# Optimization experiments

Measured on AMD Instinct MI355X. Metric: run time of the kernel, lower is better.

The kernel has to match this reference:

```python
import jax, jax.numpy as jnp
import numpy as np

N_NODES = 10000
N_EDGES = 640000
N_GRAPHS = 64
IN_FEATS = 128
H_FEATS = 128


def setup_inputs() -> dict:
    key = jax.random.key(0)
    ks = jax.random.split(key, 8)
    in_feat = jax.random.normal(ks[0], (N_NODES, IN_FEATS), dtype=jnp.float32)
    src = jax.random.randint(ks[1], (N_EDGES,), 0, N_NODES, dtype=jnp.int32)
    dst = jax.random.randint(ks[2], (N_EDGES,), 0, N_NODES, dtype=jnp.int32)
    graph_ids = jnp.sort(jax.random.randint(ks[3], (N_NODES,), 0, N_GRAPHS, dtype=jnp.int32))
    s1 = 1.0 / np.sqrt(IN_FEATS)
    s2 = 1.0 / np.sqrt(H_FEATS)
    W1 = jax.random.uniform(ks[4], (IN_FEATS, H_FEATS), jnp.float32, -s1, s1)
    b1 = jnp.zeros((H_FEATS,), jnp.float32)
    W2 = jax.random.uniform(ks[5], (H_FEATS, H_FEATS), jnp.float32, -s2, s2)
    b2 = jnp.zeros((H_FEATS,), jnp.float32)
    Wd = jax.random.uniform(ks[6], (H_FEATS, 1), jnp.float32, -s2, s2)
    bd = jnp.zeros((1,), jnp.float32)
    return {"in_feat": in_feat, "src": src, "dst": dst, "graph_ids": graph_ids,
            "W1": W1, "b1": b1, "W2": W2, "b2": b2, "Wd": Wd, "bd": bd}


def _graph_conv(x, src, dst, norm_src, norm_dst, W, b):
    # DGL GraphConv, norm='both': D_dst^{-1/2} A D_src^{-1/2} X W + b
    x = x * norm_src[:, None]
    agg = jax.ops.segment_sum(x[src], dst, num_segments=N_NODES)  # scatter-add over edges
    agg = agg * norm_dst[:, None]
    return agg @ W + b


def reference(in_feat, src, dst, graph_ids, W1, b1, W2, b2, Wd, bd):
    ones_e = jnp.ones((N_EDGES,), in_feat.dtype)
    out_deg = jax.ops.segment_sum(ones_e, src, num_segments=N_NODES)
    in_deg = jax.ops.segment_sum(ones_e, dst, num_segments=N_NODES)
    norm_src = jnp.where(out_deg > 0, out_deg, 1.0) ** -0.5
    norm_dst = jnp.where(in_deg > 0, in_deg, 1.0) ** -0.5

    h = jax.nn.relu(_graph_conv(in_feat, src, dst, norm_src, norm_dst, W1, b1))
    h = jax.nn.relu(_graph_conv(h, src, dst, norm_src, norm_dst, W2, b2))

    # dgl.mean_nodes: per-graph mean of node features
    counts = jax.ops.segment_sum(jnp.ones((N_NODES,), h.dtype), graph_ids, num_segments=N_GRAPHS)
    pooled = jax.ops.segment_sum(h, graph_ids, num_segments=N_GRAPHS)
    pooled = pooled / jnp.maximum(counts, 1.0)[:, None]

    out = pooled @ Wd + bd  # [G, 1]
    return out.squeeze(-1)
```

## Files before the change

kernel.cpp:

```cpp
#include <hip/hip_runtime.h>
#include <hip/hip_fp16.h>

#define N_NODES 10000
#define N_EDGES 640000
#define N_GRAPHS 64
#define FEATS 128

#define NSLICE 128
#define EPS (N_EDGES / NSLICE)
#define CAP 128
#define PRE_BLOCKS 1250

static inline size_t align_up(size_t x, size_t a) { return (x + a - 1) & ~(a - 1); }

__global__ __launch_bounds__(256) void hist_kernel(const int* __restrict__ src,
                                                   const int* __restrict__ dst,
                                                   unsigned short* __restrict__ counts,
                                                   unsigned short* __restrict__ scounts,
                                                   int* __restrict__ graph_cnt,
                                                   float* __restrict__ graph_sum) {
    __shared__ int h[N_NODES];
    const int tid = threadIdx.x;
    const int b = blockIdx.x;
    if (b == 0 && tid < 2 * N_GRAPHS) {
        if (tid < N_GRAPHS) graph_cnt[tid] = 0;
        else                graph_sum[tid - N_GRAPHS] = 0.f;
    }
    const bool is_dst = (b < NSLICE);
    const int slice = is_dst ? b : b - NSLICE;
    const int* col = is_dst ? dst : src;
    unsigned short* outp = (is_dst ? counts : scounts) + slice * N_NODES;

    for (int i = tid; i < N_NODES; i += 256) h[i] = 0;
    __syncthreads();
    const int4* c4 = (const int4*)(col + slice * EPS);
    for (int i = tid; i < EPS / 4; i += 256) {
        int4 v = c4[i];
        atomicAdd(&h[v.x], 1);
        atomicAdd(&h[v.y], 1);
        atomicAdd(&h[v.z], 1);
        atomicAdd(&h[v.w], 1);
    }
    __syncthreads();
    for (int i = tid; i < N_NODES; i += 256) outp[i] = (unsigned short)h[i];
}

__global__ __launch_bounds__(64) void degnorm_base_kernel(const unsigned short* __restrict__ counts,
                                                          const unsigned short* __restrict__ scounts,
                                                          const int* __restrict__ gids,
                                                          int* __restrict__ bases,
                                                          int* __restrict__ deg_in,
                                                          float* __restrict__ norm_src,
                                                          float* __restrict__ norm_dst,
                                                          int* __restrict__ graph_cnt) {
    __shared__ int gcnt[N_GRAPHS];
    const int tid = threadIdx.x;
    gcnt[tid] = 0;
    __syncthreads();
    int n = blockIdx.x * 64 + tid;
    if (n < N_NODES) {
        int run = n * CAP;
        for (int s = 0; s < NSLICE; s++) {
            int c = counts[s * N_NODES + n];
            bases[s * N_NODES + n] = run;
            run += c;
        }
        int di = run - n * CAP;
        int dou = 0;
        for (int s = 0; s < NSLICE; s++) dou += scounts[s * N_NODES + n];
        deg_in[n] = di;
        norm_dst[n] = rsqrtf((float)(di < 1 ? 1 : di));
        norm_src[n] = rsqrtf((float)(dou < 1 ? 1 : dou));
        atomicAdd(&gcnt[gids[n]], 1);
    }
    __syncthreads();
    if (gcnt[tid]) atomicAdd(&graph_cnt[tid], gcnt[tid]);
}

__global__ __launch_bounds__(256) void scatter_prescale_kernel(const int* __restrict__ src,
                                                               const int* __restrict__ dst,
                                                               const int* __restrict__ bases,
                                                               int* __restrict__ sorted_src,
                                                               const float* __restrict__ in_feat,
                                                               const float* __restrict__ norm_src,
                                                               __half* __restrict__ xs) {
    const int tid = threadIdx.x;
    if (blockIdx.x < NSLICE) {
        __shared__ int cur[N_NODES];
        const int s = blockIdx.x;
        for (int i = tid; i < N_NODES; i += 256) cur[i] = bases[s * N_NODES + i];
        __syncthreads();
        const int4* s4 = (const int4*)(src + s * EPS);
        const int4* d4 = (const int4*)(dst + s * EPS);
        for (int i = tid; i < EPS / 4; i += 256) {
            int4 sv = s4[i];
            int4 dv = d4[i];
            int p;
            p = atomicAdd(&cur[dv.x], 1); sorted_src[p] = sv.x;
            p = atomicAdd(&cur[dv.y], 1); sorted_src[p] = sv.y;
            p = atomicAdd(&cur[dv.z], 1); sorted_src[p] = sv.z;
            p = atomicAdd(&cur[dv.w], 1); sorted_src[p] = sv.w;
        }
    } else {
        int i = (blockIdx.x - NSLICE) * 256 + tid;
        if (i < N_NODES * (FEATS / 4)) {
            int n = i >> 5;
            float4 v = ((const float4*)in_feat)[i];
            float s = norm_src[n];
            __half2 h0 = __floats2half2_rn(v.x * s, v.y * s);
            __half2 h1 = __floats2half2_rn(v.z * s, v.w * s);
            __half2* o = (__half2*)(xs + (size_t)i * 4);
            o[0] = h0; o[1] = h1;
        }
    }
}

__device__ __forceinline__ void wave_aggregate(const __half* __restrict__ X,
                                               const int* __restrict__ sorted_src,
                                               const int* __restrict__ deg_in,
                                               const float* __restrict__ norm_dst,
                                               int n, int lane,
                                               float* __restrict__ As_row) {
    const int grp = lane >> 4, l16 = lane & 15;
    const int start = n * CAP;
    const int cnt = deg_in[n];
    const uint4* __restrict__ x4 = (const uint4*)X;
    float acc[8] = {0.f, 0.f, 0.f, 0.f, 0.f, 0.f, 0.f, 0.f};

    int c = grp;
    for (; c + 12 < cnt; c += 16) {
        int idx[4];
#pragma unroll
        for (int k = 0; k < 4; k++) idx[k] = sorted_src[start + c + 4 * k];
        uint4 v[4];
#pragma unroll
        for (int k = 0; k < 4; k++) v[k] = x4[idx[k] * 16 + l16];
#pragma unroll
        for (int k = 0; k < 4; k++) {
            const __half2* hp = (const __half2*)&v[k];
#pragma unroll
            for (int j = 0; j < 4; j++) {
                float2 f = __half22float2(hp[j]);
                acc[2 * j]     += f.x;
                acc[2 * j + 1] += f.y;
            }
        }
    }
    for (; c < cnt; c += 4) {
        uint4 v = x4[sorted_src[start + c] * 16 + l16];
        const __half2* hp = (const __half2*)&v;
#pragma unroll
        for (int j = 0; j < 4; j++) {
            float2 f = __half22float2(hp[j]);
            acc[2 * j]     += f.x;
            acc[2 * j + 1] += f.y;
        }
    }
#pragma unroll
    for (int j = 0; j < 8; j++) {
        acc[j] += __shfl_xor(acc[j], 16);
        acc[j] += __shfl_xor(acc[j], 32);
    }
    if (grp == 0) {
        const float nd = norm_dst[n];
        float4 f0 = make_float4(acc[0] * nd, acc[1] * nd, acc[2] * nd, acc[3] * nd);
        float4 f1 = make_float4(acc[4] * nd, acc[5] * nd, acc[6] * nd, acc[7] * nd);
        *(float4*)(As_row + l16 * 8)     = f0;
        *(float4*)(As_row + l16 * 8 + 4) = f1;
    }
}

__global__ __launch_bounds__(256) void fused_layer1_kernel(const __half* __restrict__ xs,
                                                           const int* __restrict__ sorted_src,
                                                           const int* __restrict__ deg_in,
                                                           const float* __restrict__ norm_dst,
                                                           const float* __restrict__ W,
                                                           const float* __restrict__ bias,
                                                           const float* __restrict__ scale,
                                                           __half* __restrict__ out) {
    __shared__ float As[16 * FEATS];
    const int tid = threadIdx.x;
    const int nb = blockIdx.x * 16;
    const int wave = tid >> 6, lane = tid & 63;
#pragma unroll
    for (int i = 0; i < 4; i++) {
        int ln = wave * 4 + i;
        wave_aggregate(xs, sorted_src, deg_in, norm_dst, nb + ln, lane, As + ln * FEATS);
    }
    __syncthreads();
    int fg = (tid & 31) << 2;
    int r  = tid >> 5;
    const float* a0p = As + r * FEATS;
    const float* a1p = As + (r + 8) * FEATS;
    float4 acc0 = make_float4(0.f, 0.f, 0.f, 0.f);
    float4 acc1 = make_float4(0.f, 0.f, 0.f, 0.f);
#pragma unroll 4
    for (int k = 0; k < FEATS; k++) {
        float a0 = a0p[k];
        float a1 = a1p[k];
        float4 w = *(const float4*)(W + k * FEATS + fg);
        acc0.x = fmaf(a0, w.x, acc0.x); acc0.y = fmaf(a0, w.y, acc0.y);
        acc0.z = fmaf(a0, w.z, acc0.z); acc0.w = fmaf(a0, w.w, acc0.w);
        acc1.x = fmaf(a1, w.x, acc1.x); acc1.y = fmaf(a1, w.y, acc1.y);
        acc1.z = fmaf(a1, w.z, acc1.z); acc1.w = fmaf(a1, w.w, acc1.w);
    }
    float4 bb = *(const float4*)(bias + fg);
    int gn0 = nb + r, gn1 = nb + r + 8;
    float s0 = scale[gn0], s1 = scale[gn1];
    __half2 h00 = __floats2half2_rn(fmaxf(acc0.x + bb.x, 0.f) * s0,
                                    fmaxf(acc0.y + bb.y, 0.f) * s0);
    __half2 h01 = __floats2half2_rn(fmaxf(acc0.z + bb.z, 0.f) * s0,
                                    fmaxf(acc0.w + bb.w, 0.f) * s0);
    __half2 h10 = __floats2half2_rn(fmaxf(acc1.x + bb.x, 0.f) * s1,
                                    fmaxf(acc1.y + bb.y, 0.f) * s1);
    __half2 h11 = __floats2half2_rn(fmaxf(acc1.z + bb.z, 0.f) * s1,
                                    fmaxf(acc1.w + bb.w, 0.f) * s1);
    __half2* o0 = (__half2*)(out + (size_t)gn0 * FEATS + fg);
    __half2* o1 = (__half2*)(out + (size_t)gn1 * FEATS + fg);
    o0[0] = h00; o0[1] = h01;
    o1[0] = h10; o1[1] = h11;
}

__global__ __launch_bounds__(256) void fused_layer2_kernel(const __half* __restrict__ h,
                                                           const int* __restrict__ sorted_src,
                                                           const int* __restrict__ deg_in,
                                                           const float* __restrict__ norm_dst,
                                                           const float* __restrict__ W,
                                                           const float* __restrict__ bias,
                                                           const float* __restrict__ Wd,
                                                           const int* __restrict__ gids,
                                                           float* __restrict__ graph_sum) {
    __shared__ float As[16 * FEATS];
    __shared__ float bins[N_GRAPHS];
    const int tid = threadIdx.x;
    const int nb = blockIdx.x * 16;
    const int wave = tid >> 6, lane = tid & 63;
    if (tid < N_GRAPHS) bins[tid] = 0.f;
#pragma unroll
    for (int i = 0; i < 4; i++) {
        int ln = wave * 4 + i;
        wave_aggregate(h, sorted_src, deg_in, norm_dst, nb + ln, lane, As + ln * FEATS);
    }
    __syncthreads();
    int fg = (tid & 31) << 2;
    int r  = tid >> 5;
    const float* a0p = As + r * FEATS;
    const float* a1p = As + (r + 8) * FEATS;
    float4 acc0 = make_float4(0.f, 0.f, 0.f, 0.f);
    float4 acc1 = make_float4(0.f, 0.f, 0.f, 0.f);
#pragma unroll 4
    for (int k = 0; k < FEATS; k++) {
        float a0 = a0p[k];
        float a1 = a1p[k];
        float4 w = *(const float4*)(W + k * FEATS + fg);
        acc0.x = fmaf(a0, w.x, acc0.x); acc0.y = fmaf(a0, w.y, acc0.y);
        acc0.z = fmaf(a0, w.z, acc0.z); acc0.w = fmaf(a0, w.w, acc0.w);
        acc1.x = fmaf(a1, w.x, acc1.x); acc1.y = fmaf(a1, w.y, acc1.y);
        acc1.z = fmaf(a1, w.z, acc1.z); acc1.w = fmaf(a1, w.w, acc1.w);
    }
    float4 bb = *(const float4*)(bias + fg);
    float4 wd = *(const float4*)(Wd + fg);
    float p0 = fmaxf(acc0.x + bb.x, 0.f) * wd.x + fmaxf(acc0.y + bb.y, 0.f) * wd.y +
               fmaxf(acc0.z + bb.z, 0.f) * wd.z + fmaxf(acc0.w + bb.w, 0.f) * wd.w;
    float p1 = fmaxf(acc1.x + bb.x, 0.f) * wd.x + fmaxf(acc1.y + bb.y, 0.f) * wd.y +
               fmaxf(acc1.z + bb.z, 0.f) * wd.z + fmaxf(acc1.w + bb.w, 0.f) * wd.w;
#pragma unroll
    for (int d = 16; d >= 1; d >>= 1) {
        p0 += __shfl_down(p0, d);
        p1 += __shfl_down(p1, d);
    }
    if ((tid & 31) == 0) {
        int gn0 = nb + r, gn1 = nb + r + 8;
        atomicAdd(&bins[gids[gn0]], p0);
        atomicAdd(&bins[gids[gn1]], p1);
    }
    __syncthreads();
    if (tid < N_GRAPHS) {
        float v = bins[tid];
        if (v != 0.f) atomicAdd(&graph_sum[tid], v);
    }
}

__global__ __launch_bounds__(64) void final_kernel(const float* __restrict__ graph_sum,
                                                   const int* __restrict__ graph_cnt,
                                                   const float* __restrict__ bd,
                                                   float* __restrict__ out) {
    int g = threadIdx.x;
    if (g < N_GRAPHS) {
        out[g] = graph_sum[g] / fmaxf((float)graph_cnt[g], 1.f) + bd[0];
    }
}

extern "C" void kernel_launch(void* const* d_in, const int* in_sizes, int n_in,
                              void* d_out, int out_size, void* d_ws, size_t ws_size,
                              hipStream_t stream) {
    const float* in_feat = (const float*)d_in[0];
    const int*   src     = (const int*)d_in[1];
    const int*   dst     = (const int*)d_in[2];
    const int*   gids    = (const int*)d_in[3];
    const float* W1      = (const float*)d_in[4];
    const float* b1      = (const float*)d_in[5];
    const float* W2      = (const float*)d_in[6];
    const float* b2      = (const float*)d_in[7];
    const float* Wd      = (const float*)d_in[8];
    const float* bd      = (const float*)d_in[9];
    float* out = (float*)d_out;

    char* ws = (char*)d_ws;
    size_t off = 0;
    int* graph_cnt = (int*)(ws + off); off += N_GRAPHS * 4;
    float* graph_sum = (float*)(ws + off); off += N_GRAPHS * 4;
    off = align_up(off, 512);
    unsigned short* counts  = (unsigned short*)(ws + off); off += (size_t)NSLICE * N_NODES * 2;
    off = align_up(off, 512);
    unsigned short* scounts = (unsigned short*)(ws + off); off += (size_t)NSLICE * N_NODES * 2;
    off = align_up(off, 512);
    int* bases = (int*)(ws + off); off += (size_t)NSLICE * N_NODES * 4;
    off = align_up(off, 512);
    int* deg_in  = (int*)(ws + off); off += N_NODES * 4;
    off = align_up(off, 512);
    float* norm_src = (float*)(ws + off); off += N_NODES * 4;
    off = align_up(off, 512);
    float* norm_dst = (float*)(ws + off); off += N_NODES * 4;
    off = align_up(off, 512);
    int* sorted_src = (int*)(ws + off); off += (size_t)N_NODES * CAP * 4 + 4096;
    off = align_up(off, 512);
    __half* xs   = (__half*)(ws + off); off += (size_t)N_NODES * FEATS * 2;
    off = align_up(off, 512);
    __half* h    = (__half*)(ws + off); off += (size_t)N_NODES * FEATS * 2;
    (void)ws_size;

    hist_kernel<<<2 * NSLICE, 256, 0, stream>>>(src, dst, counts, scounts,
                                                graph_cnt, graph_sum);
    degnorm_base_kernel<<<(N_NODES + 63) / 64, 64, 0, stream>>>(counts, scounts, gids,
                                                                bases, deg_in, norm_src,
                                                                norm_dst, graph_cnt);
    scatter_prescale_kernel<<<NSLICE + PRE_BLOCKS, 256, 0, stream>>>(src, dst, bases,
                                                                     sorted_src, in_feat,
                                                                     norm_src, xs);

    fused_layer1_kernel<<<N_NODES / 16, 256, 0, stream>>>(xs, sorted_src, deg_in, norm_dst,
                                                          W1, b1, norm_src, h);
    fused_layer2_kernel<<<N_NODES / 16, 256, 0, stream>>>(h, sorted_src, deg_in, norm_dst,
                                                          W2, b2, Wd, gids, graph_sum);

    final_kernel<<<1, 64, 0, stream>>>(graph_sum, graph_cnt, bd, out);
}
```

Baseline: 169.3 us.

## Replace sliced histogram CSR build with direct global-atomic bucketing

Drops the per-slice histogram, prefix-base and slice-scatter passes. Edges now go straight into fixed-capacity per-destination buckets using global atomics on padded counters, and out-degrees are counted in the same pass. The source normalisation moves out of the prescale step and into the aggregation, with rsqrt recomputed per neighbour in layer 1. Each wave now aggregates two nodes at once for more memory-level parallelism, and per-graph counts come from a binary search over the sorted graph ids. In exchange there is heavy global atomic contention, extra deg_out gathers per edge, and silent truncation if any in-degree exceeds CAP.

```diff
diff --git a/kernel.cpp b/kernel.cpp
--- a/kernel.cpp
+++ b/kernel.cpp
@@ -5,195 +5,147 @@
 #define N_EDGES 640000
 #define N_GRAPHS 64
 #define FEATS 128
-
-#define NSLICE 128
-#define EPS (N_EDGES / NSLICE)
 #define CAP 128
-#define PRE_BLOCKS 1250
+#define CSTRIDE 16
+#define NTILE (N_NODES / 16)
 
 static inline size_t align_up(size_t x, size_t a) { return (x + a - 1) & ~(a - 1); }
 
-__global__ __launch_bounds__(256) void hist_kernel(const int* __restrict__ src,
-                                                   const int* __restrict__ dst,
-                                                   unsigned short* __restrict__ counts,
-                                                   unsigned short* __restrict__ scounts,
-                                                   int* __restrict__ graph_cnt,
-                                                   float* __restrict__ graph_sum) {
-    __shared__ int h[N_NODES];
+__global__ __launch_bounds__(256) void zero_kernel(int4* __restrict__ p, int n4) {
+    int i = blockIdx.x * 256 + threadIdx.x;
+    if (i < n4) p[i] = make_int4(0, 0, 0, 0);
+}
+
+__global__ __launch_bounds__(256) void scatter_convert_kernel(const int* __restrict__ src,
+                                                              const int* __restrict__ dst,
+                                                              int* __restrict__ ctr_in,
+                                                              int* __restrict__ deg_out,
+                                                              int* __restrict__ sorted_src,
+                                                              const float* __restrict__ in_feat,
+                                                              __half* __restrict__ xs) {
     const int tid = threadIdx.x;
-    const int b = blockIdx.x;
-    if (b == 0 && tid < 2 * N_GRAPHS) {
-        if (tid < N_GRAPHS) graph_cnt[tid] = 0;
-        else                graph_sum[tid - N_GRAPHS] = 0.f;
-    }
-    const bool is_dst = (b < NSLICE);
-    const int slice = is_dst ? b : b - NSLICE;
-    const int* col = is_dst ? dst : src;
-    unsigned short* outp = (is_dst ? counts : scounts) + slice * N_NODES;
-
-    for (int i = tid; i < N_NODES; i += 256) h[i] = 0;
-    __syncthreads();
-    const int4* c4 = (const int4*)(col + slice * EPS);
-    for (int i = tid; i < EPS / 4; i += 256) {
-        int4 v = c4[i];
-        atomicAdd(&h[v.x], 1);
-        atomicAdd(&h[v.y], 1);
-        atomicAdd(&h[v.z], 1);
-        atomicAdd(&h[v.w], 1);
-    }
-    __syncthreads();
-    for (int i = tid; i < N_NODES; i += 256) outp[i] = (unsigned short)h[i];
-}
-
-__global__ __launch_bounds__(64) void degnorm_base_kernel(const unsigned short* __restrict__ counts,
-                                                          const unsigned short* __restrict__ scounts,
-                                                          const int* __restrict__ gids,
-                                                          int* __restrict__ bases,
-                                                          int* __restrict__ deg_in,
-                                                          float* __restrict__ norm_src,
-                                                          float* __restrict__ norm_dst,
-                                                          int* __restrict__ graph_cnt) {
-    __shared__ int gcnt[N_GRAPHS];
-    const int tid = threadIdx.x;
-    gcnt[tid] = 0;
-    __syncthreads();
-    int n = blockIdx.x * 64 + tid;
-    if (n < N_NODES) {
-        int run = n * CAP;
-        for (int s = 0; s < NSLICE; s++) {
-            int c = counts[s * N_NODES + n];
-            bases[s * N_NODES + n] = run;
-            run += c;
+    if (blockIdx.x < N_EDGES / 1024) {
+        const int i = blockIdx.x * 256 + tid;
+        int4 sv = ((const int4*)src)[i];
+        int4 dv = ((const int4*)dst)[i];
+        int slot;
+        slot = atomicAdd(&ctr_in[dv.x * CSTRIDE], 1);
+        if (slot < CAP) sorted_src[dv.x * CAP + slot] = sv.x;
+        atomicAdd(&deg_out[sv.x * CSTRIDE], 1);
+        slot = atomicAdd(&ctr_in[dv.y * CSTRIDE], 1);
+        if (slot < CAP) sorted_src[dv.y * CAP + slot] = sv.y;
+        atomicAdd(&deg_out[sv.y * CSTRIDE], 1);
+        slot = atomicAdd(&ctr_in[dv.z * CSTRIDE], 1);
+        if (slot < CAP) sorted_src[dv.z * CAP + slot] = sv.z;
+        atomicAdd(&deg_out[sv.z * CSTRIDE], 1);
+        slot = atomicAdd(&ctr_in[dv.w * CSTRIDE], 1);
+        if (slot < CAP) sorted_src[dv.w * CAP + slot] = sv.w;
+        atomicAdd(&deg_out[sv.w * CSTRIDE], 1);
+    } else {
+        const int i = (blockIdx.x - N_EDGES / 1024) * 256 + tid;
+        float4 v = ((const float4*)in_feat)[i];
+        __half2* o = (__half2*)(xs + (size_t)i * 4);
+        o[0] = __floats2half2_rn(v.x, v.y);
+        o[1] = __floats2half2_rn(v.z, v.w);
+    }
+}
+
+template <bool SC>
+static __device__ __forceinline__ void acc_row(uint4 v, float sc, float* a) {
+    const __half2* hp = (const __half2*)&v;
+#pragma unroll
+    for (int j = 0; j < 4; j++) {
+        float2 f = __half22float2(hp[j]);
+        if (SC) {
+            a[2 * j]     = fmaf(f.x, sc, a[2 * j]);
+            a[2 * j + 1] = fmaf(f.y, sc, a[2 * j + 1]);
+        } else {
+            a[2 * j]     += f.x;
+            a[2 * j + 1] += f.y;
         }
-        int di = run - n * CAP;
-        int dou = 0;
-        for (int s = 0; s < NSLICE; s++) dou += scounts[s * N_NODES + n];
-        deg_in[n] = di;
-        norm_dst[n] = rsqrtf((float)(di < 1 ? 1 : di));
-        norm_src[n] = rsqrtf((float)(dou < 1 ? 1 : dou));
-        atomicAdd(&gcnt[gids[n]], 1);
-    }
-    __syncthreads();
-    if (gcnt[tid]) atomicAdd(&graph_cnt[tid], gcnt[tid]);
-}
-
-__global__ __launch_bounds__(256) void scatter_prescale_kernel(const int* __restrict__ src,
-                                                               const int* __restrict__ dst,
-                                                               const int* __restrict__ bases,
-                                                               int* __restrict__ sorted_src,
-                                                               const float* __restrict__ in_feat,
-                                                               const float* __restrict__ norm_src,
-                                                               __half* __restrict__ xs) {
-    const int tid = threadIdx.x;
-    if (blockIdx.x < NSLICE) {
-        __shared__ int cur[N_NODES];
-        const int s = blockIdx.x;
-        for (int i = tid; i < N_NODES; i += 256) cur[i] = bases[s * N_NODES + i];
-        __syncthreads();
-        const int4* s4 = (const int4*)(src + s * EPS);
-        const int4* d4 = (const int4*)(dst + s * EPS);
-        for (int i = tid; i < EPS / 4; i += 256) {
-            int4 sv = s4[i];
-            int4 dv = d4[i];
-            int p;
-            p = atomicAdd(&cur[dv.x], 1); sorted_src[p] = sv.x;
-            p = atomicAdd(&cur[dv.y], 1); sorted_src[p] = sv.y;
-            p = atomicAdd(&cur[dv.z], 1); sorted_src[p] = sv.z;
-            p = atomicAdd(&cur[dv.w], 1); sorted_src[p] = sv.w;
+    }
+}
+
+template <bool SC>
+static __device__ __forceinline__ void agg_batch(const int* __restrict__ ss,
+                                                 const uint4* __restrict__ x4,
+                                                 const int* __restrict__ deg_out,
+                                                 int base, int c, int l16, float* a) {
+    int idx[4];
+#pragma unroll
+    for (int k = 0; k < 4; k++) idx[k] = ss[base + c + 4 * k];
+    uint4 v[4];
+#pragma unroll
+    for (int k = 0; k < 4; k++) v[k] = x4[idx[k] * 16 + l16];
+    float nsv[4] = {1.f, 1.f, 1.f, 1.f};
+    if (SC) {
+#pragma unroll
+        for (int k = 0; k < 4; k++) {
+            int d = deg_out[idx[k] * CSTRIDE];
+            nsv[k] = rsqrtf((float)(d < 1 ? 1 : d));
         }
-    } else {
-        int i = (blockIdx.x - NSLICE) * 256 + tid;
-        if (i < N_NODES * (FEATS / 4)) {
-            int n = i >> 5;
-            float4 v = ((const float4*)in_feat)[i];
-            float s = norm_src[n];
-            __half2 h0 = __floats2half2_rn(v.x * s, v.y * s);
-            __half2 h1 = __floats2half2_rn(v.z * s, v.w * s);
-            __half2* o = (__half2*)(xs + (size_t)i * 4);
-            o[0] = h0; o[1] = h1;
-        }
-    }
-}
-
-__device__ __forceinline__ void wave_aggregate(const __half* __restrict__ X,
-                                               const int* __restrict__ sorted_src,
-                                               const int* __restrict__ deg_in,
-                                               const float* __restrict__ norm_dst,
-                                               int n, int lane,
-                                               float* __restrict__ As_row) {
+    }
+#pragma unroll
+    for (int k = 0; k < 4; k++) acc_row<SC>(v[k], nsv[k], a);
+}
+
+template <bool SC>
+static __device__ __forceinline__ void wave_aggregate2(const __half* __restrict__ X,
+                                                       const int* __restrict__ ss,
+                                                       const int* __restrict__ ctr_in,
+                                                       const int* __restrict__ deg_out,
+                                                       int n0, int n1, int lane,
+                                                       float* __restrict__ r0,
+                                                       float* __restrict__ r1) {
     const int grp = lane >> 4, l16 = lane & 15;
-    const int start = n * CAP;
-    const int cnt = deg_in[n];
+    const int s0 = n0 * CAP, s1 = n1 * CAP;
+    const int d0 = ctr_in[n0 * CSTRIDE], d1 = ctr_in[n1 * CSTRIDE];
+    const float nd0 = rsqrtf((float)(d0 < 1 ? 1 : d0));
+    const float nd1 = rsqrtf((float)(d1 < 1 ? 1 : d1));
+    const int c0n = d0 < CAP ? d0 : CAP;
+    const int c1n = d1 < CAP ? d1 : CAP;
     const uint4* __restrict__ x4 = (const uint4*)X;
-    float acc[8] = {0.f, 0.f, 0.f, 0.f, 0.f, 0.f, 0.f, 0.f};
-
-    int c = grp;
-    for (; c + 12 < cnt; c += 16) {
-        int idx[4];
-#pragma unroll
-        for (int k = 0; k < 4; k++) idx[k] = sorted_src[start + c + 4 * k];
-        uint4 v[4];
-#pragma unroll
-        for (int k = 0; k < 4; k++) v[k] = x4[idx[k] * 16 + l16];
-#pragma unroll
-        for (int k = 0; k < 4; k++) {
-            const __half2* hp = (const __half2*)&v[k];
-#pragma unroll
-            for (int j = 0; j < 4; j++) {
-                float2 f = __half22float2(hp[j]);
-                acc[2 * j]     += f.x;
-                acc[2 * j + 1] += f.y;
-            }
-        }
-    }
-    for (; c < cnt; c += 4) {
-        uint4 v = x4[sorted_src[start + c] * 16 + l16];
-        const __half2* hp = (const __half2*)&v;
-#pragma unroll
-        for (int j = 0; j < 4; j++) {
-            float2 f = __half22float2(hp[j]);
-            acc[2 * j]     += f.x;
-            acc[2 * j + 1] += f.y;
-        }
+    float a0[8] = {0.f, 0.f, 0.f, 0.f, 0.f, 0.f, 0.f, 0.f};
+    float a1[8] = {0.f, 0.f, 0.f, 0.f, 0.f, 0.f, 0.f, 0.f};
+    int c0 = grp, c1 = grp;
+    while (c0 + 12 < c0n && c1 + 12 < c1n) {
+        agg_batch<SC>(ss, x4, deg_out, s0, c0, l16, a0);
+        agg_batch<SC>(ss, x4, deg_out, s1, c1, l16, a1);
+        c0 += 16; c1 += 16;
+    }
+    for (; c0 + 12 < c0n; c0 += 16) agg_batch<SC>(ss, x4, deg_out, s0, c0, l16, a0);
+    for (; c1 + 12 < c1n; c1 += 16) agg_batch<SC>(ss, x4, deg_out, s1, c1, l16, a1);
+    for (; c0 < c0n; c0 += 4) {
+        int idx = ss[s0 + c0];
+        float nsv = 1.f;
+        if (SC) { int d = deg_out[idx * CSTRIDE]; nsv = rsqrtf((float)(d < 1 ? 1 : d)); }
+        acc_row<SC>(x4[idx * 16 + l16], nsv, a0);
+    }
+    for (; c1 < c1n; c1 += 4) {
+        int idx = ss[s1 + c1];
+        float nsv = 1.f;
+        if (SC) { int d = deg_out[idx * CSTRIDE]; nsv = rsqrtf((float)(d < 1 ? 1 : d)); }
+        acc_row<SC>(x4[idx * 16 + l16], nsv, a1);
     }
 #pragma unroll
     for (int j = 0; j < 8; j++) {
-        acc[j] += __shfl_xor(acc[j], 16);
-        acc[j] += __shfl_xor(acc[j], 32);
+        a0[j] += __shfl_xor(a0[j], 16);
+        a0[j] += __shfl_xor(a0[j], 32);
+        a1[j] += __shfl_xor(a1[j], 16);
+        a1[j] += __shfl_xor(a1[j], 32);
     }
     if (grp == 0) {
-        const float nd = norm_dst[n];
-        float4 f0 = make_float4(acc[0] * nd, acc[1] * nd, acc[2] * nd, acc[3] * nd);
-        float4 f1 = make_float4(acc[4] * nd, acc[5] * nd, acc[6] * nd, acc[7] * nd);
-        *(float4*)(As_row + l16 * 8)     = f0;
-        *(float4*)(As_row + l16 * 8 + 4) = f1;
-    }
-}
-
-__global__ __launch_bounds__(256) void fused_layer1_kernel(const __half* __restrict__ xs,
-                                                           const int* __restrict__ sorted_src,
-                                                           const int* __restrict__ deg_in,
-                                                           const float* __restrict__ norm_dst,
-                                                           const float* __restrict__ W,
-                                                           const float* __restrict__ bias,
-                                                           const float* __restrict__ scale,
-                                                           __half* __restrict__ out) {
-    __shared__ float As[16 * FEATS];
-    const int tid = threadIdx.x;
-    const int nb = blockIdx.x * 16;
-    const int wave = tid >> 6, lane = tid & 63;
-#pragma unroll
-    for (int i = 0; i < 4; i++) {
-        int ln = wave * 4 + i;
-        wave_aggregate(xs, sorted_src, deg_in, norm_dst, nb + ln, lane, As + ln * FEATS);
-    }
-    __syncthreads();
-    int fg = (tid & 31) << 2;
-    int r  = tid >> 5;
-    const float* a0p = As + r * FEATS;
-    const float* a1p = As + (r + 8) * FEATS;
-    float4 acc0 = make_float4(0.f, 0.f, 0.f, 0.f);
-    float4 acc1 = make_float4(0.f, 0.f, 0.f, 0.f);
+        *(float4*)(r0 + l16 * 8)     = make_float4(a0[0] * nd0, a0[1] * nd0, a0[2] * nd0, a0[3] * nd0);
+        *(float4*)(r0 + l16 * 8 + 4) = make_float4(a0[4] * nd0, a0[5] * nd0, a0[6] * nd0, a0[7] * nd0);
+        *(float4*)(r1 + l16 * 8)     = make_float4(a1[0] * nd1, a1[1] * nd1, a1[2] * nd1, a1[3] * nd1);
+        *(float4*)(r1 + l16 * 8 + 4) = make_float4(a1[4] * nd1, a1[5] * nd1, a1[6] * nd1, a1[7] * nd1);
+    }
+}
+
+static __device__ __forceinline__ void gemm_2x4(const float* __restrict__ a0p,
+                                                const float* __restrict__ a1p,
+                                                const float* __restrict__ W, int fg,
+                                                float4& acc0, float4& acc1) {
 #pragma unroll 4
     for (int k = 0; k < FEATS; k++) {
         float a0 = a0p[k];
@@ -204,9 +156,36 @@
         acc1.x = fmaf(a1, w.x, acc1.x); acc1.y = fmaf(a1, w.y, acc1.y);
         acc1.z = fmaf(a1, w.z, acc1.z); acc1.w = fmaf(a1, w.w, acc1.w);
     }
+}
+
+__global__ __launch_bounds__(256) void fused_layer1_kernel(const __half* __restrict__ xs,
+                                                           const int* __restrict__ sorted_src,
+                                                           const int* __restrict__ ctr_in,
+                                                           const int* __restrict__ deg_out,
+                                                           const float* __restrict__ W,
+                                                           const float* __restrict__ bias,
+                                                           __half* __restrict__ out) {
+    __shared__ float As[16 * FEATS];
+    const int tid = threadIdx.x;
+    const int nb = blockIdx.x * 16;
+    const int wave = tid >> 6, lane = tid & 63;
+#pragma unroll
+    for (int p = 0; p < 2; p++) {
+        int ln0 = wave * 4 + 2 * p;
+        wave_aggregate2<true>(xs, sorted_src, ctr_in, deg_out, nb + ln0, nb + ln0 + 1,
+                              lane, As + ln0 * FEATS, As + (ln0 + 1) * FEATS);
+    }
+    __syncthreads();
+    const int fg = (tid & 31) << 2;
+    const int r = tid >> 5;
+    float4 acc0 = make_float4(0.f, 0.f, 0.f, 0.f);
+    float4 acc1 = make_float4(0.f, 0.f, 0.f, 0.f);
+    gemm_2x4(As + r * FEATS, As + (r + 8) * FEATS, W, fg, acc0, acc1);
     float4 bb = *(const float4*)(bias + fg);
-    int gn0 = nb + r, gn1 = nb + r + 8;
-    float s0 = scale[gn0], s1 = scale[gn1];
+    const int gn0 = nb + r, gn1 = nb + r + 8;
+    const int do0 = deg_out[gn0 * CSTRIDE], do1 = deg_out[gn1 * CSTRIDE];
+    const float s0 = rsqrtf((float)(do0 < 1 ? 1 : do0));
+    const float s1 = rsqrtf((float)(do1 < 1 ? 1 : do1));
     __half2 h00 = __floats2half2_rn(fmaxf(acc0.x + bb.x, 0.f) * s0,
                                     fmaxf(acc0.y + bb.y, 0.f) * s0);
     __half2 h01 = __floats2half2_rn(fmaxf(acc0.z + bb.z, 0.f) * s0,
@@ -221,10 +200,9 @@
     o1[0] = h10; o1[1] = h11;
 }
 
-__global__ __launch_bounds__(256) void fused_layer2_kernel(const __half* __restrict__ h,
+__global__ __launch_bounds__(256) void fused_layer2_kernel(const __half* __restrict__ hbuf,
                                                            const int* __restrict__ sorted_src,
-                                                           const int* __restrict__ deg_in,
-                                                           const float* __restrict__ norm_dst,
+                                                           const int* __restrict__ ctr_in,
                                                            const float* __restrict__ W,
                                                            const float* __restrict__ bias,
                                                            const float* __restrict__ Wd,
@@ -237,27 +215,17 @@
     const int wave = tid >> 6, lane = tid & 63;
     if (tid < N_GRAPHS) bins[tid] = 0.f;
 #pragma unroll
-    for (int i = 0; i < 4; i++) {
-        int ln = wave * 4 + i;
-        wave_aggregate(h, sorted_src, deg_in, norm_dst, nb + ln, lane, As + ln * FEATS);
+    for (int p = 0; p < 2; p++) {
+        int ln0 = wave * 4 + 2 * p;
+        wave_aggregate2<false>(hbuf, sorted_src, ctr_in, (const int*)0, nb + ln0, nb + ln0 + 1,
+                               lane, As + ln0 * FEATS, As + (ln0 + 1) * FEATS);
     }
     __syncthreads();
-    int fg = (tid & 31) << 2;
-    int r  = tid >> 5;
-    const float* a0p = As + r * FEATS;
-    const float* a1p = As + (r + 8) * FEATS;
+    const int fg = (tid & 31) << 2;
+    const int r = tid >> 5;
     float4 acc0 = make_float4(0.f, 0.f, 0.f, 0.f);
     float4 acc1 = make_float4(0.f, 0.f, 0.f, 0.f);
-#pragma unroll 4
-    for (int k = 0; k < FEATS; k++) {
-        float a0 = a0p[k];
-        float a1 = a1p[k];
-        float4 w = *(const float4*)(W + k * FEATS + fg);
-        acc0.x = fmaf(a0, w.x, acc0.x); acc0.y = fmaf(a0, w.y, acc0.y);
-        acc0.z = fmaf(a0, w.z, acc0.z); acc0.w = fmaf(a0, w.w, acc0.w);
-        acc1.x = fmaf(a1, w.x, acc1.x); acc1.y = fmaf(a1, w.y, acc1.y);
-        acc1.z = fmaf(a1, w.z, acc1.z); acc1.w = fmaf(a1, w.w, acc1.w);
-    }
+    gemm_2x4(As + r * FEATS, As + (r + 8) * FEATS, W, fg, acc0, acc1);
     float4 bb = *(const float4*)(bias + fg);
     float4 wd = *(const float4*)(Wd + fg);
     float p0 = fmaxf(acc0.x + bb.x, 0.f) * wd.x + fmaxf(acc0.y + bb.y, 0.f) * wd.y +
@@ -270,9 +238,8 @@
         p1 += __shfl_down(p1, d);
     }
     if ((tid & 31) == 0) {
-        int gn0 = nb + r, gn1 = nb + r + 8;
-        atomicAdd(&bins[gids[gn0]], p0);
-        atomicAdd(&bins[gids[gn1]], p1);
+        atomicAdd(&bins[gids[nb + r]], p0);
+        atomicAdd(&bins[gids[nb + r + 8]], p1);
     }
     __syncthreads();
     if (tid < N_GRAPHS) {
@@ -281,13 +248,23 @@
     }
 }
 
+static __device__ __forceinline__ int lower_bound_dev(const int* __restrict__ g, int key) {
+    int lo = 0, hi = N_NODES;
+    while (lo < hi) {
+        int mid = (lo + hi) >> 1;
+        if (g[mid] < key) lo = mid + 1; else hi = mid;
+    }
+    return lo;
+}
+
 __global__ __launch_bounds__(64) void final_kernel(const float* __restrict__ graph_sum,
-                                                   const int* __restrict__ graph_cnt,
+                                                   const int* __restrict__ gids,
                                                    const float* __restrict__ bd,
                                                    float* __restrict__ out) {
     int g = threadIdx.x;
     if (g < N_GRAPHS) {
-        out[g] = graph_sum[g] / fmaxf((float)graph_cnt[g], 1.f) + bd[0];
+        int cnt = lower_bound_dev(gids, g + 1) - lower_bound_dev(gids, g);
+        out[g] = graph_sum[g] / fmaxf((float)cnt, 1.f) + bd[0];
     }
 }
 
@@ -308,41 +285,27 @@
 
     char* ws = (char*)d_ws;
     size_t off = 0;
-    int* graph_cnt = (int*)(ws + off); off += N_GRAPHS * 4;
+    int* ctr_in = (int*)(ws + off);  off += (size_t)N_NODES * CSTRIDE * 4;
+    int* deg_out = (int*)(ws + off); off += (size_t)N_NODES * CSTRIDE * 4;
     float* graph_sum = (float*)(ws + off); off += N_GRAPHS * 4;
+    size_t zero_bytes = align_up(off, 16);
     off = align_up(off, 512);
-    unsigned short* counts  = (unsigned short*)(ws + off); off += (size_t)NSLICE * N_NODES * 2;
+    int* sorted_src = (int*)(ws + off); off += (size_t)N_NODES * CAP * 4;
     off = align_up(off, 512);
-    unsigned short* scounts = (unsigned short*)(ws + off); off += (size_t)NSLICE * N_NODES * 2;
+    __half* xs = (__half*)(ws + off); off += (size_t)N_NODES * FEATS * 2;
     off = align_up(off, 512);
-    int* bases = (int*)(ws + off); off += (size_t)NSLICE * N_NODES * 4;
-    off = align_up(off, 512);
-    int* deg_in  = (int*)(ws + off); off += N_NODES * 4;
-    off = align_up(off, 512);
-    float* norm_src = (float*)(ws + off); off += N_NODES * 4;
-    off = align_up(off, 512);
-    float* norm_dst = (float*)(ws + off); off += N_NODES * 4;
-    off = align_up(off, 512);
-    int* sorted_src = (int*)(ws + off); off += (size_t)N_NODES * CAP * 4 + 4096;
-    off = align_up(off, 512);
-    __half* xs   = (__half*)(ws + off); off += (size_t)N_NODES * FEATS * 2;
-    off = align_up(off, 512);
-    __half* h    = (__half*)(ws + off); off += (size_t)N_NODES * FEATS * 2;
+    __half* h  = (__half*)(ws + off); off += (size_t)N_NODES * FEATS * 2;
     (void)ws_size;
 
-    hist_kernel<<<2 * NSLICE, 256, 0, stream>>>(src, dst, counts, scounts,
-                                                graph_cnt, graph_sum);
-    degnorm_base_kernel<<<(N_NODES + 63) / 64, 64, 0, stream>>>(counts, scounts, gids,
-                                                                bases, deg_in, norm_src,
-                                                                norm_dst, graph_cnt);
-    scatter_prescale_kernel<<<NSLICE + PRE_BLOCKS, 256, 0, stream>>>(src, dst, bases,
-                                                                     sorted_src, in_feat,
-                                                                     norm_src, xs);
-
-    fused_layer1_kernel<<<N_NODES / 16, 256, 0, stream>>>(xs, sorted_src, deg_in, norm_dst,
-                                                          W1, b1, norm_src, h);
-    fused_layer2_kernel<<<N_NODES / 16, 256, 0, stream>>>(h, sorted_src, deg_in, norm_dst,
-                                                          W2, b2, Wd, gids, graph_sum);
-
-    final_kernel<<<1, 64, 0, stream>>>(graph_sum, graph_cnt, bd, out);
-}
+    const int zero_n4 = (int)(zero_bytes / 16);
+    zero_kernel<<<(zero_n4 + 255) / 256, 256, 0, stream>>>((int4*)ws, zero_n4);
+
+    scatter_convert_kernel<<<N_EDGES / 1024 + N_NODES * (FEATS / 4) / 256, 256, 0, stream>>>(
+        src, dst, ctr_in, deg_out, sorted_src, in_feat, xs);
+
+    fused_layer1_kernel<<<NTILE, 256, 0, stream>>>(xs, sorted_src, ctr_in, deg_out,
+                                                   W1, b1, h);
+    fused_layer2_kernel<<<NTILE, 256, 0, stream>>>(h, sorted_src, ctr_in,
+                                                   W2, b2, Wd, gids, graph_sum);
+    final_kernel<<<1, 64, 0, stream>>>(graph_sum, gids, bd, out);
+}
```

Result: slower. 198.0 us (+17.0%).

## Use 512-thread blocks with two interleaved node aggregations per wave

Applied to the files above, without the earlier changes.

The fused layer kernels now launch 512 threads (8 waves) per 16-node tile instead of 256. Each wave aggregates two destination nodes at once, interleaving their gather batches so more independent loads are in flight. In the GEMM stage each thread now computes one row instead of two. This aims to raise memory-level parallelism and occupancy for the gather-bound aggregation, in exchange for more per-wave register pressure and larger blocks.

```diff
diff --git a/kernel.cpp b/kernel.cpp
--- a/kernel.cpp
+++ b/kernel.cpp
@@ -10,6 +10,7 @@
 #define EPS (N_EDGES / NSLICE)
 #define CAP 128
 #define PRE_BLOCKS 1250
+#define NTILE (N_NODES / 16)
 
 static inline size_t align_up(size_t x, size_t a) { return (x + a - 1) & ~(a - 1); }
 
@@ -115,62 +116,81 @@
     }
 }
 
-__device__ __forceinline__ void wave_aggregate(const __half* __restrict__ X,
-                                               const int* __restrict__ sorted_src,
-                                               const int* __restrict__ deg_in,
-                                               const float* __restrict__ norm_dst,
-                                               int n, int lane,
-                                               float* __restrict__ As_row) {
+static __device__ __forceinline__ void acc_row(uint4 v, float* a) {
+    const __half2* hp = (const __half2*)&v;
+#pragma unroll
+    for (int j = 0; j < 4; j++) {
+        float2 f = __half22float2(hp[j]);
+        a[2 * j]     += f.x;
+        a[2 * j + 1] += f.y;
+    }
+}
+
+static __device__ __forceinline__ void agg_batch(const int* __restrict__ ss,
+                                                 const uint4* __restrict__ x4,
+                                                 int base, int c, int l16, float* a) {
+    int idx[4];
+#pragma unroll
+    for (int k = 0; k < 4; k++) idx[k] = ss[base + c + 4 * k];
+    uint4 v[4];
+#pragma unroll
+    for (int k = 0; k < 4; k++) v[k] = x4[idx[k] * 16 + l16];
+#pragma unroll
+    for (int k = 0; k < 4; k++) acc_row(v[k], a);
+}
+
+static __device__ __forceinline__ void wave_aggregate2(const __half* __restrict__ X,
+                                                       const int* __restrict__ ss,
+                                                       const int* __restrict__ deg_in,
+                                                       const float* __restrict__ nrm,
+                                                       int n0, int n1, int lane,
+                                                       float* __restrict__ r0,
+                                                       float* __restrict__ r1) {
     const int grp = lane >> 4, l16 = lane & 15;
-    const int start = n * CAP;
-    const int cnt = deg_in[n];
+    const int s0 = n0 * CAP, s1 = n1 * CAP;
+    const int c0n = deg_in[n0], c1n = deg_in[n1];
     const uint4* __restrict__ x4 = (const uint4*)X;
-    float acc[8] = {0.f, 0.f, 0.f, 0.f, 0.f, 0.f, 0.f, 0.f};
-
-    int c = grp;
-    for (; c + 12 < cnt; c += 16) {
-        int idx[4];
-#pragma unroll
-        for (int k = 0; k < 4; k++) idx[k] = sorted_src[start + c + 4 * k];
-        uint4 v[4];
-#pragma unroll
-        for (int k = 0; k < 4; k++) v[k] = x4[idx[k] * 16 + l16];
-#pragma unroll
-        for (int k = 0; k < 4; k++) {
-            const __half2* hp = (const __half2*)&v[k];
-#pragma unroll
-            for (int j = 0; j < 4; j++) {
-                float2 f = __half22float2(hp[j]);
-                acc[2 * j]     += f.x;
-                acc[2 * j + 1] += f.y;
-            }
-        }
-    }
-    for (; c < cnt; c += 4) {
-        uint4 v = x4[sorted_src[start + c] * 16 + l16];
-        const __half2* hp = (const __half2*)&v;
-#pragma unroll
-        for (int j = 0; j < 4; j++) {
-            float2 f = __half22float2(hp[j]);
-            acc[2 * j]     += f.x;
-            acc[2 * j + 1] += f.y;
-        }
-    }
+    float a0[8] = {0.f, 0.f, 0.f, 0.f, 0.f, 0.f, 0.f, 0.f};
+    float a1[8] = {0.f, 0.f, 0.f, 0.f, 0.f, 0.f, 0.f, 0.f};
+    int c0 = grp, c1 = grp;
+    while (c0 + 12 < c0n && c1 + 12 < c1n) {
+        agg_batch(ss, x4, s0, c0, l16, a0);
+        agg_batch(ss, x4, s1, c1, l16, a1);
+        c0 += 16; c1 += 16;
+    }
+    for (; c0 + 12 < c0n; c0 += 16) agg_batch(ss, x4, s0, c0, l16, a0);
+    for (; c1 + 12 < c1n; c1 += 16) agg_batch(ss, x4, s1, c1, l16, a1);
+    for (; c0 < c0n; c0 += 4) acc_row(x4[ss[s0 + c0] * 16 + l16], a0);
+    for (; c1 < c1n; c1 += 4) acc_row(x4[ss[s1 + c1] * 16 + l16], a1);
 #pragma unroll
     for (int j = 0; j < 8; j++) {
-        acc[j] += __shfl_xor(acc[j], 16);
-        acc[j] += __shfl_xor(acc[j], 32);
+        a0[j] += __shfl_xor(a0[j], 16);
+        a0[j] += __shfl_xor(a0[j], 32);
+        a1[j] += __shfl_xor(a1[j], 16);
+        a1[j] += __shfl_xor(a1[j], 32);
     }
     if (grp == 0) {
-        const float nd = norm_dst[n];
-        float4 f0 = make_float4(acc[0] * nd, acc[1] * nd, acc[2] * nd, acc[3] * nd);
-        float4 f1 = make_float4(acc[4] * nd, acc[5] * nd, acc[6] * nd, acc[7] * nd);
-        *(float4*)(As_row + l16 * 8)     = f0;
-        *(float4*)(As_row + l16 * 8 + 4) = f1;
-    }
-}
-
-__global__ __launch_bounds__(256) void fused_layer1_kernel(const __half* __restrict__ xs,
+        const float nd0 = nrm[n0], nd1 = nrm[n1];
+        *(float4*)(r0 + l16 * 8)     = make_float4(a0[0] * nd0, a0[1] * nd0, a0[2] * nd0, a0[3] * nd0);
+        *(float4*)(r0 + l16 * 8 + 4) = make_float4(a0[4] * nd0, a0[5] * nd0, a0[6] * nd0, a0[7] * nd0);
+        *(float4*)(r1 + l16 * 8)     = make_float4(a1[0] * nd1, a1[1] * nd1, a1[2] * nd1, a1[3] * nd1);
+        *(float4*)(r1 + l16 * 8 + 4) = make_float4(a1[4] * nd1, a1[5] * nd1, a1[6] * nd1, a1[7] * nd1);
+    }
+}
+
+static __device__ __forceinline__ void gemm_1x4(const float* __restrict__ ap,
+                                                const float* __restrict__ W, int fg,
+                                                float4& acc) {
+#pragma unroll 4
+    for (int k = 0; k < FEATS; k++) {
+        float a = ap[k];
+        float4 w = *(const float4*)(W + k * FEATS + fg);
+        acc.x = fmaf(a, w.x, acc.x); acc.y = fmaf(a, w.y, acc.y);
+        acc.z = fmaf(a, w.z, acc.z); acc.w = fmaf(a, w.w, acc.w);
+    }
+}
+
+__global__ __launch_bounds__(512) void fused_layer1_kernel(const __half* __restrict__ xs,
                                                            const int* __restrict__ sorted_src,
                                                            const int* __restrict__ deg_in,
                                                            const float* __restrict__ norm_dst,
@@ -182,46 +202,26 @@
     const int tid = threadIdx.x;
     const int nb = blockIdx.x * 16;
     const int wave = tid >> 6, lane = tid & 63;
-#pragma unroll
-    for (int i = 0; i < 4; i++) {
-        int ln = wave * 4 + i;
-        wave_aggregate(xs, sorted_src, deg_in, norm_dst, nb + ln, lane, As + ln * FEATS);
-    }
-    __syncthreads();
-    int fg = (tid & 31) << 2;
-    int r  = tid >> 5;
-    const float* a0p = As + r * FEATS;
-    const float* a1p = As + (r + 8) * FEATS;
-    float4 acc0 = make_float4(0.f, 0.f, 0.f, 0.f);
-    float4 acc1 = make_float4(0.f, 0.f, 0.f, 0.f);
-#pragma unroll 4
-    for (int k = 0; k < FEATS; k++) {
-        float a0 = a0p[k];
-        float a1 = a1p[k];
-        float4 w = *(const float4*)(W + k * FEATS + fg);
-        acc0.x = fmaf(a0, w.x, acc0.x); acc0.y = fmaf(a0, w.y, acc0.y);
-        acc0.z = fmaf(a0, w.z, acc0.z); acc0.w = fmaf(a0, w.w, acc0.w);
-        acc1.x = fmaf(a1, w.x, acc1.x); acc1.y = fmaf(a1, w.y, acc1.y);
-        acc1.z = fmaf(a1, w.z, acc1.z); acc1.w = fmaf(a1, w.w, acc1.w);
-    }
+    const int ln0 = wave * 2;
+    wave_aggregate2(xs, sorted_src, deg_in, norm_dst, nb + ln0, nb + ln0 + 1,
+                    lane, As + ln0 * FEATS, As + (ln0 + 1) * FEATS);
+    __syncthreads();
+    const int fg = (tid & 31) << 2;
+    const int r = tid >> 5;
+    float4 acc = make_float4(0.f, 0.f, 0.f, 0.f);
+    gemm_1x4(As + r * FEATS, W, fg, acc);
     float4 bb = *(const float4*)(bias + fg);
-    int gn0 = nb + r, gn1 = nb + r + 8;
-    float s0 = scale[gn0], s1 = scale[gn1];
-    __half2 h00 = __floats2half2_rn(fmaxf(acc0.x + bb.x, 0.f) * s0,
-                                    fmaxf(acc0.y + bb.y, 0.f) * s0);
-    __half2 h01 = __floats2half2_rn(fmaxf(acc0.z + bb.z, 0.f) * s0,
-                                    fmaxf(acc0.w + bb.w, 0.f) * s0);
-    __half2 h10 = __floats2half2_rn(fmaxf(acc1.x + bb.x, 0.f) * s1,
-                                    fmaxf(acc1.y + bb.y, 0.f) * s1);
-    __half2 h11 = __floats2half2_rn(fmaxf(acc1.z + bb.z, 0.f) * s1,
-                                    fmaxf(acc1.w + bb.w, 0.f) * s1);
-    __half2* o0 = (__half2*)(out + (size_t)gn0 * FEATS + fg);
-    __half2* o1 = (__half2*)(out + (size_t)gn1 * FEATS + fg);
-    o0[0] = h00; o0[1] = h01;
-    o1[0] = h10; o1[1] = h11;
-}
-
-__global__ __launch_bounds__(256) void fused_layer2_kernel(const __half* __restrict__ h,
+    const int gn = nb + r;
+    const float s = scale[gn];
+    __half2 h0 = __floats2half2_rn(fmaxf(acc.x + bb.x, 0.f) * s,
+                                   fmaxf(acc.y + bb.y, 0.f) * s);
+    __half2 h1 = __floats2half2_rn(fmaxf(acc.z + bb.z, 0.f) * s,
+                                   fmaxf(acc.w + bb.w, 0.f) * s);
+    __half2* o = (__half2*)(out + (size_t)gn * FEATS + fg);
+    o[0] = h0; o[1] = h1;
+}
+
+__global__ __launch_bounds__(512) void fused_layer2_kernel(const __half* __restrict__ hbuf,
                                                            const int* __restrict__ sorted_src,
                                                            const int* __restrict__ deg_in,
                                                            const float* __restrict__ norm_dst,
@@ -236,44 +236,21 @@
     const int nb = blockIdx.x * 16;
     const int wave = tid >> 6, lane = tid & 63;
     if (tid < N_GRAPHS) bins[tid] = 0.f;
-#pragma unroll
-    for (int i = 0; i < 4; i++) {
-        int ln = wave * 4 + i;
-        wave_aggregate(h, sorted_src, deg_in, norm_dst, nb + ln, lane, As + ln * FEATS);
-    }
-    __syncthreads();
-    int fg = (tid & 31) << 2;
-    int r  = tid >> 5;
-    const float* a0p = As + r * FEATS;
-    const float* a1p = As + (r + 8) * FEATS;
-    float4 acc0 = make_float4(0.f, 0.f, 0.f, 0.f);
-    float4 acc1 = make_float4(0.f, 0.f, 0.f, 0.f);
-#pragma unroll 4
-    for (int k = 0; k < FEATS; k++) {
-        float a0 = a0p[k];
-        float a1 = a1p[k];
-        float4 w = *(const float4*)(W + k * FEATS + fg);
-        acc0.x = fmaf(a0, w.x, acc0.x); acc0.y = fmaf(a0, w.y, acc0.y);
-        acc0.z = fmaf(a0, w.z, acc0.z); acc0.w = fmaf(a0, w.w, acc0.w);
-        acc1.x = fmaf(a1, w.x, acc1.x); acc1.y = fmaf(a1, w.y, acc1.y);
-        acc1.z = fmaf(a1, w.z, acc1.z); acc1.w = fmaf(a1, w.w, acc1.w);
-    }
+    const int ln0 = wave * 2;
+    wave_aggregate2(hbuf, sorted_src, deg_in, norm_dst, nb + ln0, nb + ln0 + 1,
+                    lane, As + ln0 * FEATS, As + (ln0 + 1) * FEATS);
+    __syncthreads();
+    const int fg = (tid & 31) << 2;
+    const int r = tid >> 5;
+    float4 acc = make_float4(0.f, 0.f, 0.f, 0.f);
+    gemm_1x4(As + r * FEATS, W, fg, acc);
     float4 bb = *(const float4*)(bias + fg);
     float4 wd = *(const float4*)(Wd + fg);
-    float p0 = fmaxf(acc0.x + bb.x, 0.f) * wd.x + fmaxf(acc0.y + bb.y, 0.f) * wd.y +
-               fmaxf(acc0.z + bb.z, 0.f) * wd.z + fmaxf(acc0.w + bb.w, 0.f) * wd.w;
-    float p1 = fmaxf(acc1.x + bb.x, 0.f) * wd.x + fmaxf(acc1.y + bb.y, 0.f) * wd.y +
-               fmaxf(acc1.z + bb.z, 0.f) * wd.z + fmaxf(acc1.w + bb.w, 0.f) * wd.w;
-#pragma unroll
-    for (int d = 16; d >= 1; d >>= 1) {
-        p0 += __shfl_down(p0, d);
-        p1 += __shfl_down(p1, d);
-    }
-    if ((tid & 31) == 0) {
-        int gn0 = nb + r, gn1 = nb + r + 8;
-        atomicAdd(&bins[gids[gn0]], p0);
-        atomicAdd(&bins[gids[gn1]], p1);
-    }
+    float p0 = fmaxf(acc.x + bb.x, 0.f) * wd.x + fmaxf(acc.y + bb.y, 0.f) * wd.y +
+               fmaxf(acc.z + bb.z, 0.f) * wd.z + fmaxf(acc.w + bb.w, 0.f) * wd.w;
+#pragma unroll
+    for (int d = 16; d >= 1; d >>= 1) p0 += __shfl_down(p0, d);
+    if ((tid & 31) == 0) atomicAdd(&bins[gids[nb + r]], p0);
     __syncthreads();
     if (tid < N_GRAPHS) {
         float v = bins[tid];
@@ -325,9 +302,9 @@
     off = align_up(off, 512);
     int* sorted_src = (int*)(ws + off); off += (size_t)N_NODES * CAP * 4 + 4096;
     off = align_up(off, 512);
-    __half* xs   = (__half*)(ws + off); off += (size_t)N_NODES * FEATS * 2;
-    off = align_up(off, 512);
-    __half* h    = (__half*)(ws + off); off += (size_t)N_NODES * FEATS * 2;
+    __half* xs = (__half*)(ws + off); off += (size_t)N_NODES * FEATS * 2;
+    off = align_up(off, 512);
+    __half* h  = (__half*)(ws + off); off += (size_t)N_NODES * FEATS * 2;
     (void)ws_size;
 
     hist_kernel<<<2 * NSLICE, 256, 0, stream>>>(src, dst, counts, scounts,
@@ -339,10 +316,10 @@
                                                                      sorted_src, in_feat,
                                                                      norm_src, xs);
 
-    fused_layer1_kernel<<<N_NODES / 16, 256, 0, stream>>>(xs, sorted_src, deg_in, norm_dst,
-                                                          W1, b1, norm_src, h);
-    fused_layer2_kernel<<<N_NODES / 16, 256, 0, stream>>>(h, sorted_src, deg_in, norm_dst,
-                                                          W2, b2, Wd, gids, graph_sum);
+    fused_layer1_kernel<<<NTILE, 512, 0, stream>>>(xs, sorted_src, deg_in, norm_dst,
+                                                   W1, b1, norm_src, h);
+    fused_layer2_kernel<<<NTILE, 512, 0, stream>>>(h, sorted_src, deg_in, norm_dst,
+                                                   W2, b2, Wd, gids, graph_sum);
 
     final_kernel<<<1, 64, 0, stream>>>(graph_sum, graph_cnt, bd, out);
 }
```

Measured after the change: 181.3 us. 1.07x slower.
